# Performance work log

Measured on AMD Instinct MI355X. Metric: run time of the kernel, lower is better.

Reference implementation:

```python
import jax, jax.numpy as jnp
import numpy as np
from jax import lax
from jax.scipy.special import ndtr

EV = 6           # even context kernel size
K = 3            # num_mixtures
GROUPS = 3       # grouped 1x1 convs (grps=3 for clrchs<3)
SCALE_MIN = 0.11 # lower bound on mixture std
LP = 257         # 257 CDF sampling points (8-bit Y/RGB path)


def _cdf_pts():
    # cdf_sampling_pts__Y_RGB from __init__
    pts = jnp.linspace(-127.5, 128.5, LP) / 255.0
    pts = pts.at[0].set(-147.5 / 255.0).at[-1].set(148.5 / 255.0)
    return pts.astype(jnp.float32)


def _conv(x, w, b, groups=1):
    y = lax.conv_general_dilated(
        x, w, window_strides=(1, 1), padding='VALID',
        dimension_numbers=('NCHW', 'OIHW', 'NCHW'),
        feature_group_count=groups)
    return y + b[None, :, None, None]


def _forward_float(y_condition, W0, b0, W1, b1, W2, b2):
    # replicate pad: paddd0_00_11 = (Ev//2-1, Ev//2, Ev//2-1, Ev//2)
    y = jnp.pad(y_condition, ((0, 0), (0, 0), (EV // 2 - 1, EV // 2), (EV // 2 - 1, EV // 2)), mode='edge')
    h = jax.nn.relu(_conv(y, W0, b0, groups=1))        # [B, 192, H, W]
    h = jax.nn.relu(_conv(h, W1, b1, groups=GROUPS))   # [B, 192, H, W]
    p = _conv(h, W2, b2, groups=GROUPS)                # [B, 9, H, W] GMM params
    B, _, H, W = p.shape
    p = p.reshape(B, 3, K, H, W)                       # param-major: mu / raw_scale / raw_weight
    mu, sr, wr = p[:, 0], p[:, 1], p[:, 2]             # each [B, K, H, W]
    scale = jnp.maximum(jnp.exp(sr), SCALE_MIN)
    wts = jax.nn.softmax(wr, axis=1)                   # mixture weights over K
    t = _cdf_pts()                                     # [LP]
    z = (t - mu[..., None]) / scale[..., None]         # [B, K, H, W, LP]
    cdf = jnp.einsum('bkhw,bkhwl->bhwl', wts, ndtr(z)) # mixture CDF, [B, H, W, LP]
    return jnp.clip(cdf, 0.0, 1.0 - 1e-6)


def setup_inputs() -> dict:
    key = jax.random.key(0)
    ks = jax.random.split(key, 4)
    return {
        'y_condition': jax.random.uniform(ks[0], (1, 1, 256, 256), jnp.float32),
        'W0': jax.random.normal(ks[1], (192, 1, EV, EV), jnp.float32) * 0.05,
        'b0': jnp.zeros((192,), jnp.float32),
        'W1': jax.random.normal(ks[2], (192, 64, 1, 1), jnp.float32) * 0.05,
        'b1': jnp.zeros((192,), jnp.float32),
        'W2': jax.random.normal(ks[3], (9, 64, 1, 1), jnp.float32) * 0.05,
        'b2': jnp.zeros((9,), jnp.float32),
    }


def reference(y_condition, W0, b0, W1, b1, W2, b2):
    cdf_f = _forward_float(y_condition, W0, b0, W1, b1, W2, b2)
    # _convert_to_int_and_normalize with needs_normalization=True
    new_max = jnp.float32(2 ** 16 - (LP - 1))
    cdf_i = jnp.round(cdf_f * new_max).astype(jnp.int16)
    cdf_i = cdf_i + jnp.arange(LP, dtype=jnp.int16)
    return cdf_i
```

## Files before the change

kernel.cpp:

```cpp
#include <hip/hip_runtime.h>
#include <math.h>

#define LPTS 257
#define NPIX 65536
#define PPB  32
#define SW   68


__device__ __forceinline__ float xla_exp32(float x)
{
#pragma clang fp contract(off)
    x = fminf(x, 88.3762626647950f);
    x = fmaxf(x, -87.3365478515625f);
    const float m = floorf(fmaf(x, 1.44269504088896341f, 0.5f));
    float r = fmaf(m, -0.693359375f, x);
    r = fmaf(m, 2.12194440e-4f, r);
    const float r2 = r * r;
    float p = 1.9875691500e-4f;
    p = fmaf(p, r, 1.3981999507e-3f);
    p = fmaf(p, r, 8.3334519073e-3f);
    p = fmaf(p, r, 4.1665795894e-2f);
    p = fmaf(p, r, 1.6666665459e-1f);
    p = fmaf(p, r, 5.0000001201e-1f);
    float y = fmaf(p, r2, r) + 1.0f;
    const int e = (int)m;
    const float s = __int_as_float((e + 127) << 23);
    return y * s;
}

__device__ __forceinline__ float ieee_div(float n, float d)
{
    const float r0 = __builtin_amdgcn_rcpf(d);
    const float e  = fmaf(-d, r0, 1.0f);
    const float r1 = fmaf(e, r0, r0);
    const float q0 = n * r1;
    const float e1 = fmaf(-d, q0, n);
    const float q1 = fmaf(e1, r1, q0);
    const float e2 = fmaf(-d, q1, n);
    return fmaf(e2, r1, q1);
}

__device__ __forceinline__ float xla_erf32(float x)
{
#pragma clang fp contract(off)
    x = fminf(fmaxf(x, -4.0f), 4.0f);
    const float x2 = x * x;
    float pa = -2.72614225801306e-10f;
    pa = fmaf(pa, x2, 2.77068142495902e-08f);
    pa = fmaf(pa, x2, -2.10102402082508e-06f);
    pa = fmaf(pa, x2, -5.69250639462346e-05f);
    pa = fmaf(pa, x2, -7.34990630326855e-04f);
    pa = fmaf(pa, x2, -2.95459980854025e-03f);
    pa = fmaf(pa, x2, -1.60960333262415e-02f);
    float pb = -1.45660718464996e-05f;
    pb = fmaf(pb, x2, -2.13374055278905e-04f);
    pb = fmaf(pb, x2, -1.68282697438203e-03f);
    pb = fmaf(pb, x2, -7.37332916720468e-03f);
    pb = fmaf(pb, x2, -1.42647390514189e-02f);
    return ieee_div(x * pa, pb);
}

__device__ __forceinline__ float xla_erfc_ge1(float x)
{
#pragma clang fp contract(off)
    const float z = xla_exp32(-(x * x));
    const float q = 1.0f / x;
    const float y2 = q * q;
    float p;
    if (x < 2.0f) {
        p = 2.326819970068386e-02f;
        p = fmaf(p, y2, -1.387039388740657e-01f);
        p = fmaf(p, y2, 3.687424674597105e-01f);
        p = fmaf(p, y2, -5.824733027278666e-01f);
        p = fmaf(p, y2, 6.210004621745983e-01f);
        p = fmaf(p, y2, -4.944515323274145e-01f);
        p = fmaf(p, y2, 3.404879937665872e-01f);
        p = fmaf(p, y2, -2.741127028184656e-01f);
        p = fmaf(p, y2, 5.638259427386472e-01f);
    } else {
        p = -1.047766399936249e+01f;
        p = fmaf(p, y2, 1.297719955372516e+01f);
        p = fmaf(p, y2, -7.495518717768503e+00f);
        p = fmaf(p, y2, 2.921019019210786e+00f);
        p = fmaf(p, y2, -1.015265279202700e+00f);
        p = fmaf(p, y2, 4.218463358204948e-01f);
        p = fmaf(p, y2, -2.820767439740514e-01f);
        p = fmaf(p, y2, 5.641895067754075e-01f);
    }
    return z * q * p;
}

__device__ __forceinline__ void xla_ndtr3_y(
    float z0, float z1, float z2, float& o0, float& o1, float& o2)
{
#pragma clang fp contract(off)
    const float c = __uint_as_float(0x3f3504f3u);
    const float w0 = z0 * c, w1 = z1 * c, w2 = z2 * c;
    const float a0 = fabsf(w0), a1 = fabsf(w1), a2 = fabsf(w2);

    const float E0 = xla_erf32(w0);
    const float E1 = xla_erf32(w1);
    const float E2 = xla_erf32(w2);

    const float m0 = 1.0f - fabsf(E0);
    const float m1 = 1.0f - fabsf(E1);
    const float m2 = 1.0f - fabsf(E2);

    float y0 = (a0 < c) ? (1.0f + E0) : ((w0 > 0.0f) ? (2.0f - m0) : m0);
    float y1 = (a1 < c) ? (1.0f + E1) : ((w1 > 0.0f) ? (2.0f - m1) : m1);
    float y2 = (a2 < c) ? (1.0f + E2) : ((w2 > 0.0f) ? (2.0f - m2) : m2);

    const float amax = fmaxf(fmaxf(a0, a1), a2);
    if (__builtin_expect(__ballot(amax > 1.0f) != 0ull, 0)) {
        {
            const float ec = xla_erfc_ge1(a0);
            const float yc = (w0 > 0.0f) ? (2.0f - ec) : ec;
            y0 = (a0 > 1.0f) ? yc : y0;
        }
        {
            const float ec = xla_erfc_ge1(a1);
            const float yc = (w1 > 0.0f) ? (2.0f - ec) : ec;
            y1 = (a1 > 1.0f) ? yc : y1;
        }
        {
            const float ec = xla_erfc_ge1(a2);
            const float yc = (w2 > 0.0f) ? (2.0f - ec) : ec;
            y2 = (a2 > 1.0f) ? yc : y2;
        }
    }
    o0 = y0; o1 = y1; o2 = y2;
}

__device__ __forceinline__ float xla_ndtr32(float zf)
{
#pragma clang fp contract(off)
    const float c = __uint_as_float(0x3f3504f3u);
    const float w = zf * c;
    const float aw = fabsf(w);
    const float E = xla_erf32(w);
    const float e_mid = 1.0f - fabsf(E);
    float y = (aw < c) ? (1.0f + E)
                       : ((w > 0.0f) ? (2.0f - e_mid) : e_mid);
    if (__builtin_expect(__ballot(aw > 1.0f) != 0ull, 0)) {
        const float ec = xla_erfc_ge1(aw);
        const float yc = (w > 0.0f) ? (2.0f - ec) : ec;
        y = (aw > 1.0f) ? yc : y;
    }
    return 0.5f * y;
}

__device__ __forceinline__ int quantize(float cdf, int l)
{
    int r = (int)rintf(cdf * 65280.0f);
    r = r > 32767 ? 32767 : r;
    r = r < -32768 ? -32768 : r;
    return (int)((short)(r + l));
}

__global__ __launch_bounds__(256) void entropy_params(
    const float* __restrict__ y,
    const float* __restrict__ W0, const float* __restrict__ b0,
    const float* __restrict__ W1, const float* __restrict__ b1,
    const float* __restrict__ W2, const float* __restrict__ b2,
    float* __restrict__ prm_g)
{
#pragma clang fp contract(off)
    __shared__ __align__(16) float tile[13][16];
    __shared__ __align__(16) float w0s[64 * 36];
    __shared__ __align__(16) float w1s[64 * SW];
    __shared__ __align__(16) float w2t[64 * 4];
    __shared__ __align__(16) float b0s[64];
    __shared__ __align__(16) float b1s[64];
    __shared__ float b2s[3];
    __shared__ __align__(16) float h0s[64 * SW];

    const int bx  = blockIdx.x & 31;
    const int by  = blockIdx.x >> 5;
    const int g   = blockIdx.y;
    const int tid = threadIdx.x;
    const int p   = tid >> 2;
    const int t   = tid & 3;
    const int py  = p >> 3;
    const int px  = p & 7;

    {
        const float4* src = (const float4*)(W0 + g * 2304);
        for (int i = tid; i < 576; i += 256) ((float4*)w0s)[i] = src[i];
    }
    {
        const float4* src = (const float4*)(W1 + g * 4096);
        for (int i4 = tid; i4 < 1024; i4 += 256) {
            const float4 v = src[i4];
            const int c2 = i4 >> 4;
            const int k4 = (i4 & 15) << 2;
            *(float4*)&w1s[c2 * SW + k4] = v;
        }
    }
    if (tid < 64) {
        w2t[tid * 4 + 0] = W2[(3 * g + 0) * 64 + tid];
        w2t[tid * 4 + 1] = W2[(3 * g + 1) * 64 + tid];
        w2t[tid * 4 + 2] = W2[(3 * g + 2) * 64 + tid];
        w2t[tid * 4 + 3] = 0.0f;
    } else if (tid < 128) {
        b0s[tid - 64] = b0[g * 64 + (tid - 64)];
    } else if (tid < 192) {
        b1s[tid - 128] = b1[g * 64 + (tid - 128)];
    }
    if (tid < 3) b2s[tid] = b2[3 * g + tid];

    if (tid < 169) {
        const int rr = tid / 13;
        const int cc = tid - rr * 13;
        int gy = by * 8 - 2 + rr;  gy = gy < 0 ? 0 : (gy > 255 ? 255 : gy);
        int gx = bx * 8 - 2 + cc;  gx = gx < 0 ? 0 : (gx > 255 ? 255 : gx);
        tile[rr][cc] = y[gy * 256 + gx];
    }
    __syncthreads();

    float patch[36];
#pragma unroll
    for (int i = 0; i < 6; ++i)
#pragma unroll
        for (int j = 0; j < 6; ++j)
            patch[i * 6 + j] = tile[py + i][px + j];

    float h[16];
#pragma unroll
    for (int j = 0; j < 16; ++j) h[j] = 0.0f;
#pragma unroll
    for (int q = 0; q < 9; ++q) {
        const float pk0 = patch[4 * q + 0];
        const float pk1 = patch[4 * q + 1];
        const float pk2 = patch[4 * q + 2];
        const float pk3 = patch[4 * q + 3];
#pragma unroll
        for (int j = 0; j < 16; ++j) {
            const int c1 = t + 4 * j;
            const float4 wv = *(const float4*)&w0s[c1 * 36 + 4 * q];
            h[j] = fmaf(wv.x, pk0, h[j]);
            h[j] = fmaf(wv.y, pk1, h[j]);
            h[j] = fmaf(wv.z, pk2, h[j]);
            h[j] = fmaf(wv.w, pk3, h[j]);
        }
    }
#pragma unroll
    for (int j = 0; j < 16; ++j) {
        const int c1 = t + 4 * j;
        h0s[p * SW + c1] = fmaxf(h[j] + b0s[c1], 0.0f);
    }
    __syncthreads();

    float a2[16];
#pragma unroll
    for (int j = 0; j < 16; ++j) a2[j] = 0.0f;
#pragma unroll
    for (int k = 0; k < 16; ++k) {
        const float4 hv = *(const float4*)&h0s[p * SW + 4 * k];
#pragma unroll
        for (int j = 0; j < 16; ++j) {
            const int c2 = t + 4 * j;
            const float4 wv = *(const float4*)&w1s[c2 * SW + 4 * k];
            a2[j] = fmaf(wv.x, hv.x, a2[j]);
            a2[j] = fmaf(wv.y, hv.y, a2[j]);
            a2[j] = fmaf(wv.z, hv.z, a2[j]);
            a2[j] = fmaf(wv.w, hv.w, a2[j]);
        }
    }
    __syncthreads();
#pragma unroll
    for (int j = 0; j < 16; ++j) {
        const int c2 = t + 4 * j;
        h0s[p * SW + c2] = fmaxf(a2[j] + b1s[c2], 0.0f);
    }
    __syncthreads();

    if (t == 0) {
        float p0 = 0.0f, p1 = 0.0f, p2 = 0.0f;
#pragma unroll
        for (int k = 0; k < 16; ++k) {
            const float4 hv = *(const float4*)&h0s[p * SW + 4 * k];
            const float hva[4] = {hv.x, hv.y, hv.z, hv.w};
#pragma unroll
            for (int i = 0; i < 4; ++i) {
                const float4 wv = *(const float4*)&w2t[(4 * k + i) * 4];
                p0 = fmaf(wv.x, hva[i], p0);
                p1 = fmaf(wv.y, hva[i], p1);
                p2 = fmaf(wv.z, hva[i], p2);
            }
        }
        p0 += b2s[0]; p1 += b2s[1]; p2 += b2s[2];

        const int pix = (by * 8 + py) * 256 + bx * 8 + px;

        if (g == 0) {
            prm_g[0 * NPIX + pix] = p0;
            prm_g[1 * NPIX + pix] = p1;
            prm_g[2 * NPIX + pix] = p2;
        } else if (g == 1) {
            const float s0 = fmaxf(xla_exp32(p0), 0.11f);
            const float s1 = fmaxf(xla_exp32(p1), 0.11f);
            const float s2 = fmaxf(xla_exp32(p2), 0.11f);
            prm_g[3 * NPIX + pix] = s0;
            prm_g[4 * NPIX + pix] = s1;
            prm_g[5 * NPIX + pix] = s2;
            prm_g[6 * NPIX + pix] = 1.0f / s0;
            prm_g[7 * NPIX + pix] = 1.0f / s1;
            prm_g[8 * NPIX + pix] = 1.0f / s2;
        } else {
            const float m  = fmaxf(fmaxf(p0, p1), p2);
            const float e0 = xla_exp32(p0 - m);
            const float e1 = xla_exp32(p1 - m);
            const float e2 = xla_exp32(p2 - m);
            const float s  = (e0 + e1) + e2;
            prm_g[ 9 * NPIX + pix] = 0.5f * (e0 / s);
            prm_g[10 * NPIX + pix] = 0.5f * (e1 / s);
            prm_g[11 * NPIX + pix] = 0.5f * (e2 / s);
        }
    }
}

__global__ __launch_bounds__(256) void entropy_cdf(
    const float* __restrict__ prm_g,
    int* __restrict__ out)
{
#pragma clang fp contract(off)
    __shared__ __align__(16) float prm[PPB][12];

    const int base = blockIdx.x * PPB;
    const int tid  = threadIdx.x;

    for (int i = tid; i < 12 * PPB; i += 256) {
        const int j = i >> 5;
        const int p = i & 31;
        prm[p][j] = prm_g[j * NPIX + base + p];
    }
    __syncthreads();

    const float CLIP = (float)(1.0 - 1e-6);

    {
        const int l = tid;
        const float t32 = (l == 0)
            ? (float)(-147.5 / 255.0)
            : (float)((((double)l) - 127.5) / 255.0);
#pragma unroll 4
        for (int p = 0; p < PPB; ++p) {
            const float4 v0 = *(const float4*)&prm[p][0];
            const float4 v1 = *(const float4*)&prm[p][4];
            const float4 v2 = *(const float4*)&prm[p][8];

            const float x0 = t32 - v0.x;
            const float x1 = t32 - v0.y;
            const float x2 = t32 - v0.z;
            const float qa = x0 * v1.z;
            const float qb = x1 * v1.w;
            const float qc = x2 * v2.x;
            const float ra = fmaf(-v0.w, qa, x0);
            const float rb = fmaf(-v1.x, qb, x1);
            const float rc = fmaf(-v1.y, qc, x2);
            const float z0 = fmaf(ra, v1.z, qa);
            const float z1 = fmaf(rb, v1.w, qb);
            const float z2 = fmaf(rc, v2.x, qc);

            float y0, y1, y2;
            xla_ndtr3_y(z0, z1, z2, y0, y1, y2);

            float cdf = fmaf(v2.w, y2, fmaf(v2.z, y1, v2.y * y0));
            cdf = fminf(fmaxf(cdf, 0.0f), CLIP);

            out[(size_t)(base + p) * LPTS + l] = quantize(cdf, l);
        }
    }

    if (tid < PPB) {
        const int p = tid;
        const float t32 = (float)(148.5 / 255.0);
        const float4 v0 = *(const float4*)&prm[p][0];
        const float4 v1 = *(const float4*)&prm[p][4];
        const float4 v2 = *(const float4*)&prm[p][8];

        const float x0 = t32 - v0.x;
        const float x1 = t32 - v0.y;
        const float x2 = t32 - v0.z;
        const float qa = x0 * v1.z;
        const float qb = x1 * v1.w;
        const float qc = x2 * v2.x;
        const float ra = fmaf(-v0.w, qa, x0);
        const float rb = fmaf(-v1.x, qb, x1);
        const float rc = fmaf(-v1.y, qc, x2);
        const float z0 = fmaf(ra, v1.z, qa);
        const float z1 = fmaf(rb, v1.w, qb);
        const float z2 = fmaf(rc, v2.x, qc);

        float y0, y1, y2;
        xla_ndtr3_y(z0, z1, z2, y0, y1, y2);

        float cdf = fmaf(v2.w, y2, fmaf(v2.z, y1, v2.y * y0));
        cdf = fminf(fmaxf(cdf, 0.0f), CLIP);

        out[(size_t)(base + p) * LPTS + 256] = quantize(cdf, 256);
    }
}

__global__ __launch_bounds__(256) void entropy_fused(
    const float* __restrict__ y,
    const float* __restrict__ W0, const float* __restrict__ b0,
    const float* __restrict__ W1, const float* __restrict__ b1,
    const float* __restrict__ W2, const float* __restrict__ b2,
    int* __restrict__ out)
{
#pragma clang fp contract(off)

    __shared__ float tile[21][22];
    __shared__ float prm[9][257];

    const int bx  = blockIdx.x & 15;
    const int by  = blockIdx.x >> 4;
    const int tid = threadIdx.x;
    const int tx  = tid & 15;
    const int ty  = tid >> 4;

    for (int idx = tid; idx < 21 * 21; idx += 256) {
        const int r = idx / 21;
        const int c = idx - r * 21;
        int gy = by * 16 - 2 + r; gy = gy < 0 ? 0 : (gy > 255 ? 255 : gy);
        int gx = bx * 16 - 2 + c; gx = gx < 0 ? 0 : (gx > 255 ? 255 : gx);
        tile[r][c] = y[gy * 256 + gx];
    }
    __syncthreads();

    float patch[36];
#pragma unroll
    for (int i = 0; i < 6; ++i)
#pragma unroll
        for (int j = 0; j < 6; ++j)
            patch[i * 6 + j] = tile[ty + i][tx + j];

    for (int g = 0; g < 3; ++g) {
        float h0[64];
#pragma unroll
        for (int c = 0; c < 64; ++c) {
            float acc = 0.0f;
            const float* w = W0 + (g * 64 + c) * 36;
#pragma unroll
            for (int k = 0; k < 36; ++k)
                acc = fmaf(w[k], patch[k], acc);
            acc = acc + b0[g * 64 + c];
            h0[c] = fmaxf(acc, 0.0f);
        }

        float p0 = 0.0f, p1 = 0.0f, p2 = 0.0f;
#pragma unroll 2
        for (int c = 0; c < 64; ++c) {
            float acc = 0.0f;
            const float* w = W1 + (g * 64 + c) * 64;
#pragma unroll
            for (int j = 0; j < 64; ++j)
                acc = fmaf(w[j], h0[j], acc);
            acc = acc + b1[g * 64 + c];
            acc = fmaxf(acc, 0.0f);
            p0 = fmaf(W2[(3 * g + 0) * 64 + c], acc, p0);
            p1 = fmaf(W2[(3 * g + 1) * 64 + c], acc, p1);
            p2 = fmaf(W2[(3 * g + 2) * 64 + c], acc, p2);
        }
        p0 = p0 + b2[3 * g + 0];
        p1 = p1 + b2[3 * g + 1];
        p2 = p2 + b2[3 * g + 2];

        if (g == 0) {
            prm[0][tid] = p0; prm[1][tid] = p1; prm[2][tid] = p2;
        } else if (g == 1) {
            prm[3][tid] = fmaxf(xla_exp32(p0), 0.11f);
            prm[4][tid] = fmaxf(xla_exp32(p1), 0.11f);
            prm[5][tid] = fmaxf(xla_exp32(p2), 0.11f);
        } else {
            const float m  = fmaxf(fmaxf(p0, p1), p2);
            const float e0 = xla_exp32(p0 - m);
            const float e1 = xla_exp32(p1 - m);
            const float e2 = xla_exp32(p2 - m);
            const float s  = (e0 + e1) + e2;
            prm[6][tid] = e0 / s;
            prm[7][tid] = e1 / s;
            prm[8][tid] = e2 / s;
        }
    }
    __syncthreads();

    const int rowbase = (by * 16) * 256 + bx * 16;
    const float CLIP = (float)(1.0 - 1e-6);

    {
        const int l = tid;
        const float t32 = (l == 0)
            ? (float)(-147.5 / 255.0)
            : (float)((((double)l) - 127.5) / 255.0);
        for (int p = 0; p < 256; ++p) {
            const float mu0 = prm[0][p], mu1 = prm[1][p], mu2 = prm[2][p];
            const float sc0 = prm[3][p], sc1 = prm[4][p], sc2 = prm[5][p];
            const float w0  = prm[6][p], w1  = prm[7][p], w2  = prm[8][p];

            const float n0 = xla_ndtr32((t32 - mu0) / sc0);
            const float n1 = xla_ndtr32((t32 - mu1) / sc1);
            const float n2 = xla_ndtr32((t32 - mu2) / sc2);

            float cdf = fmaf(w2, n2, fmaf(w1, n1, w0 * n0));
            cdf = fminf(fmaxf(cdf, 0.0f), CLIP);

            const int pix = rowbase + (p >> 4) * 256 + (p & 15);
            out[(size_t)pix * LPTS + l] = quantize(cdf, l);
        }
    }

    {
        const int p = tid;
        const float t32 = (float)(148.5 / 255.0);
        const float mu0 = prm[0][p], mu1 = prm[1][p], mu2 = prm[2][p];
        const float sc0 = prm[3][p], sc1 = prm[4][p], sc2 = prm[5][p];
        const float w0  = prm[6][p], w1  = prm[7][p], w2  = prm[8][p];

        const float n0 = xla_ndtr32((t32 - mu0) / sc0);
        const float n1 = xla_ndtr32((t32 - mu1) / sc1);
        const float n2 = xla_ndtr32((t32 - mu2) / sc2);

        float cdf = fmaf(w2, n2, fmaf(w1, n1, w0 * n0));
        cdf = fminf(fmaxf(cdf, 0.0f), CLIP);

        const int pix = rowbase + (p >> 4) * 256 + (p & 15);
        out[(size_t)pix * LPTS + 256] = quantize(cdf, 256);
    }
}

extern "C" void kernel_launch(void* const* d_in, const int* in_sizes, int n_in,
                              void* d_out, int out_size, void* d_ws, size_t ws_size,
                              hipStream_t stream)
{
    const float* y  = (const float*)d_in[0];
    const float* W0 = (const float*)d_in[1];
    const float* b0 = (const float*)d_in[2];
    const float* W1 = (const float*)d_in[3];
    const float* b1 = (const float*)d_in[4];
    const float* W2 = (const float*)d_in[5];
    const float* b2 = (const float*)d_in[6];

    int* out = (int*)d_out;

    const size_t need = (size_t)12 * NPIX * sizeof(float);
    if (d_ws != nullptr && ws_size >= need) {
        float* prm_g = (float*)d_ws;
        entropy_params<<<dim3(1024, 3), dim3(256), 0, stream>>>(
            y, W0, b0, W1, b1, W2, b2, prm_g);
        entropy_cdf<<<dim3(NPIX / PPB), dim3(256), 0, stream>>>(prm_g, out);
    } else {
        entropy_fused<<<dim3(256), dim3(256), 0, stream>>>(
            y, W0, b0, W1, b1, W2, b2, out);
    }
}
```

Baseline: 180.2 us.

## Remap conv-net threads to compute two vertically adjacent pixels each

Each thread now handles 8 channels for two vertically adjacent pixels instead of 16 channels for one pixel, so every weight float4 read from shared memory is reused across two pixels. A 7x6 patch is held so the two overlapping 6x6 windows share registers. The intent is to halve shared-memory weight traffic per FMA in the 6x6 conv and the grouped 1x1 conv. The final 1x1 stage is now done by only 32 threads (t==0), each looping over two pixels, which serializes that tail work.

```diff
diff --git a/kernel.cpp b/kernel.cpp
--- a/kernel.cpp
+++ b/kernel.cpp
@@ -178,10 +178,12 @@
     const int by  = blockIdx.x >> 5;
     const int g   = blockIdx.y;
     const int tid = threadIdx.x;
-    const int p   = tid >> 2;
-    const int t   = tid & 3;
-    const int py  = p >> 3;
-    const int px  = p & 7;
+    const int pq  = tid >> 3;
+    const int t   = tid & 7;
+    const int sy  = pq >> 3;
+    const int sx  = pq & 7;
+    const int pA  = (2 * sy) * 8 + sx;
+    const int pB  = pA + 8;
 
     {
         const float4* src = (const float4*)(W0 + g * 2304);
@@ -217,104 +219,118 @@
     }
     __syncthreads();
 
-    float patch[36];
-#pragma unroll
-    for (int i = 0; i < 6; ++i)
+    float pr[7][6];
+#pragma unroll
+    for (int i = 0; i < 7; ++i)
 #pragma unroll
         for (int j = 0; j < 6; ++j)
-            patch[i * 6 + j] = tile[py + i][px + j];
-
-    float h[16];
-#pragma unroll
-    for (int j = 0; j < 16; ++j) h[j] = 0.0f;
-#pragma unroll
-    for (int q = 0; q < 9; ++q) {
-        const float pk0 = patch[4 * q + 0];
-        const float pk1 = patch[4 * q + 1];
-        const float pk2 = patch[4 * q + 2];
-        const float pk3 = patch[4 * q + 3];
-#pragma unroll
-        for (int j = 0; j < 16; ++j) {
-            const int c1 = t + 4 * j;
-            const float4 wv = *(const float4*)&w0s[c1 * 36 + 4 * q];
-            h[j] = fmaf(wv.x, pk0, h[j]);
-            h[j] = fmaf(wv.y, pk1, h[j]);
-            h[j] = fmaf(wv.z, pk2, h[j]);
-            h[j] = fmaf(wv.w, pk3, h[j]);
-        }
-    }
-#pragma unroll
-    for (int j = 0; j < 16; ++j) {
-        const int c1 = t + 4 * j;
-        h0s[p * SW + c1] = fmaxf(h[j] + b0s[c1], 0.0f);
-    }
-    __syncthreads();
-
-    float a2[16];
-#pragma unroll
-    for (int j = 0; j < 16; ++j) a2[j] = 0.0f;
+            pr[i][j] = tile[2 * sy + i][sx + j];
+
+#pragma unroll
+    for (int j = 0; j < 8; ++j) {
+        const int c1 = t + 8 * j;
+        const float* wr = w0s + c1 * 36;
+        float ha = 0.0f, hb = 0.0f;
+#pragma unroll
+        for (int q = 0; q < 9; ++q) {
+            const float4 wv = *(const float4*)&wr[4 * q];
+            const int k0 = 4 * q;
+            const int ki0 = k0 / 6,      kj0 = k0 - ki0 * 6;
+            const int ki1 = (k0+1) / 6,  kj1 = (k0+1) - ki1 * 6;
+            const int ki2 = (k0+2) / 6,  kj2 = (k0+2) - ki2 * 6;
+            const int ki3 = (k0+3) / 6,  kj3 = (k0+3) - ki3 * 6;
+            ha = fmaf(wv.x, pr[ki0][kj0], ha);
+            ha = fmaf(wv.y, pr[ki1][kj1], ha);
+            ha = fmaf(wv.z, pr[ki2][kj2], ha);
+            ha = fmaf(wv.w, pr[ki3][kj3], ha);
+            hb = fmaf(wv.x, pr[ki0 + 1][kj0], hb);
+            hb = fmaf(wv.y, pr[ki1 + 1][kj1], hb);
+            hb = fmaf(wv.z, pr[ki2 + 1][kj2], hb);
+            hb = fmaf(wv.w, pr[ki3 + 1][kj3], hb);
+        }
+        const float bb = b0s[c1];
+        h0s[pA * SW + c1] = fmaxf(ha + bb, 0.0f);
+        h0s[pB * SW + c1] = fmaxf(hb + bb, 0.0f);
+    }
+    __syncthreads();
+
+    float aA[8], aB[8];
+#pragma unroll
+    for (int j = 0; j < 8; ++j) { aA[j] = 0.0f; aB[j] = 0.0f; }
 #pragma unroll
     for (int k = 0; k < 16; ++k) {
-        const float4 hv = *(const float4*)&h0s[p * SW + 4 * k];
-#pragma unroll
-        for (int j = 0; j < 16; ++j) {
-            const int c2 = t + 4 * j;
-            const float4 wv = *(const float4*)&w1s[c2 * SW + 4 * k];
-            a2[j] = fmaf(wv.x, hv.x, a2[j]);
-            a2[j] = fmaf(wv.y, hv.y, a2[j]);
-            a2[j] = fmaf(wv.z, hv.z, a2[j]);
-            a2[j] = fmaf(wv.w, hv.w, a2[j]);
-        }
-    }
-    __syncthreads();
-#pragma unroll
-    for (int j = 0; j < 16; ++j) {
-        const int c2 = t + 4 * j;
-        h0s[p * SW + c2] = fmaxf(a2[j] + b1s[c2], 0.0f);
+        const float4 hvA = *(const float4*)&h0s[pA * SW + 4 * k];
+        const float4 hvB = *(const float4*)&h0s[pB * SW + 4 * k];
+#pragma unroll
+        for (int j = 0; j < 8; ++j) {
+            const float4 wv = *(const float4*)&w1s[(t + 8 * j) * SW + 4 * k];
+            aA[j] = fmaf(wv.x, hvA.x, aA[j]);
+            aA[j] = fmaf(wv.y, hvA.y, aA[j]);
+            aA[j] = fmaf(wv.z, hvA.z, aA[j]);
+            aA[j] = fmaf(wv.w, hvA.w, aA[j]);
+            aB[j] = fmaf(wv.x, hvB.x, aB[j]);
+            aB[j] = fmaf(wv.y, hvB.y, aB[j]);
+            aB[j] = fmaf(wv.z, hvB.z, aB[j]);
+            aB[j] = fmaf(wv.w, hvB.w, aB[j]);
+        }
+    }
+    __syncthreads();
+#pragma unroll
+    for (int j = 0; j < 8; ++j) {
+        const int c2 = t + 8 * j;
+        const float bb = b1s[c2];
+        h0s[pA * SW + c2] = fmaxf(aA[j] + bb, 0.0f);
+        h0s[pB * SW + c2] = fmaxf(aB[j] + bb, 0.0f);
     }
     __syncthreads();
 
     if (t == 0) {
-        float p0 = 0.0f, p1 = 0.0f, p2 = 0.0f;
-#pragma unroll
-        for (int k = 0; k < 16; ++k) {
-            const float4 hv = *(const float4*)&h0s[p * SW + 4 * k];
-            const float hva[4] = {hv.x, hv.y, hv.z, hv.w};
-#pragma unroll
-            for (int i = 0; i < 4; ++i) {
-                const float4 wv = *(const float4*)&w2t[(4 * k + i) * 4];
-                p0 = fmaf(wv.x, hva[i], p0);
-                p1 = fmaf(wv.y, hva[i], p1);
-                p2 = fmaf(wv.z, hva[i], p2);
+#pragma unroll
+        for (int sel = 0; sel < 2; ++sel) {
+            const int p = sel ? pB : pA;
+            float p0 = 0.0f, p1 = 0.0f, p2 = 0.0f;
+#pragma unroll
+            for (int k = 0; k < 16; ++k) {
+                const float4 hv = *(const float4*)&h0s[p * SW + 4 * k];
+                const float hva[4] = {hv.x, hv.y, hv.z, hv.w};
+#pragma unroll
+                for (int i = 0; i < 4; ++i) {
+                    const float4 wv = *(const float4*)&w2t[(4 * k + i) * 4];
+                    p0 = fmaf(wv.x, hva[i], p0);
+                    p1 = fmaf(wv.y, hva[i], p1);
+                    p2 = fmaf(wv.z, hva[i], p2);
+                }
             }
-        }
-        p0 += b2s[0]; p1 += b2s[1]; p2 += b2s[2];
-
-        const int pix = (by * 8 + py) * 256 + bx * 8 + px;
-
-        if (g == 0) {
-            prm_g[0 * NPIX + pix] = p0;
-            prm_g[1 * NPIX + pix] = p1;
-            prm_g[2 * NPIX + pix] = p2;
-        } else if (g == 1) {
-            const float s0 = fmaxf(xla_exp32(p0), 0.11f);
-            const float s1 = fmaxf(xla_exp32(p1), 0.11f);
-            const float s2 = fmaxf(xla_exp32(p2), 0.11f);
-            prm_g[3 * NPIX + pix] = s0;
-            prm_g[4 * NPIX + pix] = s1;
-            prm_g[5 * NPIX + pix] = s2;
-            prm_g[6 * NPIX + pix] = 1.0f / s0;
-            prm_g[7 * NPIX + pix] = 1.0f / s1;
-            prm_g[8 * NPIX + pix] = 1.0f / s2;
-        } else {
-            const float m  = fmaxf(fmaxf(p0, p1), p2);
-            const float e0 = xla_exp32(p0 - m);
-            const float e1 = xla_exp32(p1 - m);
-            const float e2 = xla_exp32(p2 - m);
-            const float s  = (e0 + e1) + e2;
-            prm_g[ 9 * NPIX + pix] = 0.5f * (e0 / s);
-            prm_g[10 * NPIX + pix] = 0.5f * (e1 / s);
-            prm_g[11 * NPIX + pix] = 0.5f * (e2 / s);
+            p0 += b2s[0]; p1 += b2s[1]; p2 += b2s[2];
+
+            const int py = p >> 3;
+            const int px = p & 7;
+            const int pix = (by * 8 + py) * 256 + bx * 8 + px;
+
+            if (g == 0) {
+                prm_g[0 * NPIX + pix] = p0;
+                prm_g[1 * NPIX + pix] = p1;
+                prm_g[2 * NPIX + pix] = p2;
+            } else if (g == 1) {
+                const float s0 = fmaxf(xla_exp32(p0), 0.11f);
+                const float s1 = fmaxf(xla_exp32(p1), 0.11f);
+                const float s2 = fmaxf(xla_exp32(p2), 0.11f);
+                prm_g[3 * NPIX + pix] = s0;
+                prm_g[4 * NPIX + pix] = s1;
+                prm_g[5 * NPIX + pix] = s2;
+                prm_g[6 * NPIX + pix] = 1.0f / s0;
+                prm_g[7 * NPIX + pix] = 1.0f / s1;
+                prm_g[8 * NPIX + pix] = 1.0f / s2;
+            } else {
+                const float m  = fmaxf(fmaxf(p0, p1), p2);
+                const float e0 = xla_exp32(p0 - m);
+                const float e1 = xla_exp32(p1 - m);
+                const float e2 = xla_exp32(p2 - m);
+                const float s  = (e0 + e1) + e2;
+                prm_g[ 9 * NPIX + pix] = 0.5f * (e0 / s);
+                prm_g[10 * NPIX + pix] = 0.5f * (e1 / s);
+                prm_g[11 * NPIX + pix] = 0.5f * (e2 / s);
+            }
         }
     }
 }
```

Result: no change. 180.0 us (-0.1%).
